# Kernel optimization log

Measured on AMD Instinct MI355X. Metric: run time of the kernel, lower is better.

Reference implementation:

```python
import jax, jax.numpy as jnp
import numpy as np
from jax import lax


def _pairwise_dist(a, b):
    # a: (T, D), b: (T, D) -> (T, T) Euclidean distances via GEMM trick
    a2 = jnp.sum(a * a, axis=-1)
    b2 = jnp.sum(b * b, axis=-1)
    sq = a2[:, None] + b2[None, :] - 2.0 * (a @ b.T)
    return jnp.sqrt(jnp.maximum(sq, 1e-12))


def _frechet(seq1, seq2):
    cost = _pairwise_dist(seq1, seq2)  # (T, T)
    ca0 = lax.cummax(cost[0])          # first row boundary: running max

    def row_step(prev, cost_row):
        # prev: ca[i-1, :]; cost_row: cost[i, :]
        c0 = jnp.maximum(prev[0], cost_row[0])  # first-column boundary

        def col_step(left, x):
            c, up, diag = x
            val = jnp.maximum(c, jnp.minimum(jnp.minimum(up, left), diag))
            return val, val

        _, rest = lax.scan(col_step, c0, (cost_row[1:], prev[1:], prev[:-1]))
        cur = jnp.concatenate([c0[None], rest])
        return cur, None

    final_row, _ = lax.scan(row_step, ca0, cost[1:])
    return final_row[-1]


def setup_inputs() -> dict:
    key = jax.random.key(0)
    k1, k2 = jax.random.split(key)
    B, T, D = 32, 1024, 64
    pred = jax.random.normal(k1, (B, T, D), dtype=jnp.float32)
    targ = jax.random.normal(k2, (B, T, D), dtype=jnp.float32)
    return {"pred": pred, "targ": targ}


def reference(pred, targ):
    dists = jax.vmap(_frechet)(pred, targ)  # (B,)
    return jnp.mean(dists)
```

## Files before the change

kernel.cpp:

```cpp
#include <hip/hip_runtime.h>
#include <hip/hip_bf16.h>

#define T_LEN 1024
#define D_DIM 64
#define BATCH 32

__global__ __launch_bounds__(256) void cost_kernel(const float* __restrict__ pred,
                                                   const float* __restrict__ targ,
                                                   float* __restrict__ cost) {
    const int b = blockIdx.z;
    const float* P = pred + (size_t)b * T_LEN * D_DIM;
    const float* T = targ + (size_t)b * T_LEN * D_DIM;
    float* C = cost + (size_t)b * T_LEN * T_LEN;
    const int row0 = blockIdx.y * 64;
    const int col0 = blockIdx.x * 64;

    __shared__ __align__(16) float ps[64][68];
    __shared__ __align__(16) float ts[64][68];
    __shared__ float p2[64], t2[64];

    const int tid = threadIdx.x;

#pragma unroll
    for (int it = 0; it < 4; it++) {
        int f = tid + 256 * it;
        int row = f >> 4;
        int kc = f & 15;
        float4 v = *(const float4*)(P + (size_t)(row0 + row) * D_DIM + 4 * kc);
        ps[4 * kc + 0][row] = v.x; ps[4 * kc + 1][row] = v.y;
        ps[4 * kc + 2][row] = v.z; ps[4 * kc + 3][row] = v.w;
        float4 w = *(const float4*)(T + (size_t)(col0 + row) * D_DIM + 4 * kc);
        ts[4 * kc + 0][row] = w.x; ts[4 * kc + 1][row] = w.y;
        ts[4 * kc + 2][row] = w.z; ts[4 * kc + 3][row] = w.w;
    }
    __syncthreads();

    if (tid < 128) {
        int idx = tid & 63;
        float s = 0.0f;
        if (tid < 64) {
#pragma unroll
            for (int k = 0; k < 64; k++) { float x = ps[k][idx]; s += x * x; }
            p2[idx] = s;
        } else {
#pragma unroll
            for (int k = 0; k < 64; k++) { float x = ts[k][idx]; s += x * x; }
            t2[idx] = s;
        }
    }
    __syncthreads();

    const int tx = tid & 15, ty = tid >> 4;
    const int r0 = 4 * ty, c0 = 4 * tx;
    float acc[4][4];
#pragma unroll
    for (int i = 0; i < 4; i++)
#pragma unroll
        for (int j = 0; j < 4; j++) acc[i][j] = 0.0f;

#pragma unroll 8
    for (int k = 0; k < 64; k++) {
        float4 a = *(const float4*)&ps[k][r0];
        float4 bb = *(const float4*)&ts[k][c0];
        float av[4] = {a.x, a.y, a.z, a.w};
        float bv[4] = {bb.x, bb.y, bb.z, bb.w};
#pragma unroll
        for (int i = 0; i < 4; i++)
#pragma unroll
            for (int j = 0; j < 4; j++) acc[i][j] += av[i] * bv[j];
    }

#pragma unroll
    for (int i = 0; i < 4; i++) {
        float4 o;
        float pa = p2[r0 + i];
        float d0 = pa + t2[c0 + 0] - 2.0f * acc[i][0];
        float d1 = pa + t2[c0 + 1] - 2.0f * acc[i][1];
        float d2 = pa + t2[c0 + 2] - 2.0f * acc[i][2];
        float d3 = pa + t2[c0 + 3] - 2.0f * acc[i][3];
        o.x = sqrtf(fmaxf(d0, 1e-12f));
        o.y = sqrtf(fmaxf(d1, 1e-12f));
        o.z = sqrtf(fmaxf(d2, 1e-12f));
        o.w = sqrtf(fmaxf(d3, 1e-12f));
        *(float4*)(C + (size_t)(row0 + r0 + i) * T_LEN + (col0 + c0)) = o;
    }
}

#define PD 8
__global__ __launch_bounds__(64) void dp_kernel(const float* __restrict__ cost,
                                                float* __restrict__ out) {
    const int b = blockIdx.x;
    const int t = threadIdx.x;
    const float INF = __builtin_inff();
    const float* C = cost + (size_t)b * T_LEN * T_LEN + 16 * t;

    float prev[16];
#pragma unroll
    for (int j = 0; j < 16; j++) prev[j] = INF;
    float right_out = INF;
    float diag_feed = INF;

    float4 pipe[PD][4];
#pragma unroll
    for (int d = 0; d < PD; d++) {
        int r = d - t; r = r < 0 ? 0 : (r > T_LEN - 1 ? T_LEN - 1 : r);
        const float4* p = (const float4*)(C + (size_t)r * T_LEN);
        pipe[d][0] = p[0]; pipe[d][1] = p[1]; pipe[d][2] = p[2]; pipe[d][3] = p[3];
    }

    const int S = T_LEN + 63;
    const int NCH = (S + PD - 1) / PD;
    int s = 0;
    for (int chunk = 0; chunk < NCH; chunk++) {
#pragma unroll
        for (int u = 0; u < PD; u++, s++) {
            int r = s - t;
            float inc = __shfl_up(right_out, 1, 64);
            float left = inc, diag = diag_feed;
            diag_feed = inc;
            if (t == 0) { left = (r == 0) ? -INF : INF; diag = INF; }
            if (r >= 0 && r < T_LEN) {
                const float* cb = (const float*)&pipe[u][0];
#pragma unroll
                for (int j = 0; j < 16; j++) {
                    float c = cb[j];
                    float up = prev[j];
                    float v = fmaxf(c, fminf(fminf(up, diag), left));
                    diag = up; left = v; prev[j] = v;
                }
                right_out = left;
            }
            int rn = s + PD - t; rn = rn < 0 ? 0 : (rn > T_LEN - 1 ? T_LEN - 1 : rn);
            const float4* p = (const float4*)(C + (size_t)rn * T_LEN);
            pipe[u][0] = p[0]; pipe[u][1] = p[1]; pipe[u][2] = p[2]; pipe[u][3] = p[3];
        }
    }
    if (t == 63) atomicAdd(out, prev[15] * (1.0f / (float)BATCH));
}

__global__ __launch_bounds__(64) void dp_fused_kernel(const float* __restrict__ pred,
                                                      const float* __restrict__ targ,
                                                      float* __restrict__ out) {
    const int b = blockIdx.x;
    const int t = threadIdx.x;
    const float INF = __builtin_inff();
    const float* P = pred + (size_t)b * T_LEN * D_DIM;
    const float* T = targ + (size_t)b * T_LEN * D_DIM + (size_t)(16 * t) * D_DIM;

    float prev[16];
#pragma unroll
    for (int j = 0; j < 16; j++) prev[j] = INF;
    float right_out = INF;
    float diag_feed = INF;

    for (int s = 0; s < T_LEN + 63; s++) {
        int r = s - t;
        float inc = __shfl_up(right_out, 1, 64);
        float left = inc, diag = diag_feed;
        diag_feed = inc;
        if (t == 0) { left = (r == 0) ? -INF : INF; diag = INF; }
        if (r >= 0 && r < T_LEN) {
            float4 pr[16];
            const float4* pp = (const float4*)(P + (size_t)r * D_DIM);
#pragma unroll
            for (int q = 0; q < 16; q++) pr[q] = pp[q];
#pragma unroll
            for (int j = 0; j < 16; j++) {
                const float4* tp = (const float4*)(T + (size_t)j * D_DIM);
                float acc = 0.0f;
#pragma unroll
                for (int q = 0; q < 16; q++) {
                    float4 tv = tp[q];
                    float dx = pr[q].x - tv.x; acc += dx * dx;
                    float dy = pr[q].y - tv.y; acc += dy * dy;
                    float dz = pr[q].z - tv.z; acc += dz * dz;
                    float dw = pr[q].w - tv.w; acc += dw * dw;
                }
                float c = sqrtf(fmaxf(acc, 1e-12f));
                float up = prev[j];
                float v = fmaxf(c, fminf(fminf(up, diag), left));
                diag = up; left = v; prev[j] = v;
            }
            right_out = left;
        }
    }
    if (t == 63) atomicAdd(out, prev[15] * (1.0f / (float)BATCH));
}

extern "C" void kernel_launch(void* const* d_in, const int* in_sizes, int n_in,
                              void* d_out, int out_size, void* d_ws, size_t ws_size,
                              hipStream_t stream) {
    const float* pred = (const float*)d_in[0];
    const float* targ = (const float*)d_in[1];
    float* out = (float*)d_out;

    hipMemsetAsync(out, 0, sizeof(float) * out_size, stream);

    const size_t per_batch = (size_t)T_LEN * T_LEN * sizeof(float);
    int bpg = (int)(ws_size / per_batch);
    if (bpg > BATCH) bpg = BATCH;

    if (bpg >= 1) {
        float* cost = (float*)d_ws;
        for (int g0 = 0; g0 < BATCH; g0 += bpg) {
            int gb = (BATCH - g0) < bpg ? (BATCH - g0) : bpg;
            dim3 grid(16, 16, gb);
            cost_kernel<<<grid, 256, 0, stream>>>(pred + (size_t)g0 * T_LEN * D_DIM,
                                                  targ + (size_t)g0 * T_LEN * D_DIM,
                                                  cost);
            dp_kernel<<<gb, 64, 0, stream>>>(cost, out);
        }
    } else {
        dp_fused_kernel<<<BATCH, 64, 0, stream>>>(pred, targ, out);
    }
}
```

Before: 309.8 us.

## Pad cost matrix with INF slack rows to remove DP boundary branches

The cost workspace is laid out with INF-filled slack rows before and after each batch, so the wavefront DP kernel can run every step without clamping row indices or checking validity. The per-cell recurrence is rewritten with fmed3 to use fewer min/max operations. The cost GEMM moves to 128x128 tiles with 8x8 register blocking and a two-chunk K loop. The cost is an extra fill kernel, a larger workspace requirement, and more register pressure in the cost kernel.

```diff
diff --git a/kernel.cpp b/kernel.cpp
--- a/kernel.cpp
+++ b/kernel.cpp
@@ -1,94 +1,188 @@
 #include <hip/hip_runtime.h>
 #include <hip/hip_bf16.h>
+#include <math.h>
 
 #define T_LEN 1024
 #define D_DIM 64
 #define BATCH 32
 
+#define SLACK_FRONT 64
+#define SLACK_BACK  72
+#define ROW_STRIDE  (T_LEN + SLACK_FRONT)
+#define PD 8
+
+__global__ __launch_bounds__(256) void fill_slack_kernel(float* __restrict__ ws) {
+    int g = blockIdx.x * 256 + threadIdx.x;
+    int b = g >> 14;
+    int off = g & 16383;
+    float4* dst = (float4*)(ws + (size_t)b * (ROW_STRIDE * T_LEN)) + off;
+    const float INF = __builtin_inff();
+    *dst = make_float4(INF, INF, INF, INF);
+}
+
 __global__ __launch_bounds__(256) void cost_kernel(const float* __restrict__ pred,
                                                    const float* __restrict__ targ,
-                                                   float* __restrict__ cost) {
+                                                   float* __restrict__ cost_base,
+                                                   unsigned long long batch_stride_f) {
     const int b = blockIdx.z;
     const float* P = pred + (size_t)b * T_LEN * D_DIM;
     const float* T = targ + (size_t)b * T_LEN * D_DIM;
-    float* C = cost + (size_t)b * T_LEN * T_LEN;
-    const int row0 = blockIdx.y * 64;
-    const int col0 = blockIdx.x * 64;
-
-    __shared__ __align__(16) float ps[64][68];
-    __shared__ __align__(16) float ts[64][68];
-    __shared__ float p2[64], t2[64];
+    float* C = cost_base + (size_t)b * batch_stride_f;
+    const int row0 = blockIdx.y * 128;
+    const int col0 = blockIdx.x * 128;
+
+    __shared__ __align__(16) float ps[32][132];
+    __shared__ __align__(16) float ts[32][132];
+    __shared__ float p2[128], t2[128];
 
     const int tid = threadIdx.x;
 
-#pragma unroll
-    for (int it = 0; it < 4; it++) {
-        int f = tid + 256 * it;
-        int row = f >> 4;
-        int kc = f & 15;
-        float4 v = *(const float4*)(P + (size_t)(row0 + row) * D_DIM + 4 * kc);
-        ps[4 * kc + 0][row] = v.x; ps[4 * kc + 1][row] = v.y;
-        ps[4 * kc + 2][row] = v.z; ps[4 * kc + 3][row] = v.w;
-        float4 w = *(const float4*)(T + (size_t)(col0 + row) * D_DIM + 4 * kc);
-        ts[4 * kc + 0][row] = w.x; ts[4 * kc + 1][row] = w.y;
-        ts[4 * kc + 2][row] = w.z; ts[4 * kc + 3][row] = w.w;
+    {
+        int r = tid & 127;
+        const float* src = (tid < 128) ? (P + (size_t)(row0 + r) * D_DIM)
+                                       : (T + (size_t)(col0 + r) * D_DIM);
+        float s = 0.0f;
+#pragma unroll
+        for (int q = 0; q < 16; q++) {
+            float4 v = ((const float4*)src)[q];
+            s += v.x * v.x + v.y * v.y + v.z * v.z + v.w * v.w;
+        }
+        if (tid < 128) p2[r] = s; else t2[r] = s;
+    }
+
+    const int lane = tid & 63, wv = tid >> 6;
+    const int TX = (lane & 7) + 8 * (wv & 1);
+    const int TY = (lane >> 3) + 8 * (wv >> 1);
+
+    float acc[8][8];
+#pragma unroll
+    for (int i = 0; i < 8; i++)
+#pragma unroll
+        for (int j = 0; j < 8; j++) acc[i][j] = 0.0f;
+
+#pragma unroll
+    for (int chunk = 0; chunk < 2; ++chunk) {
+        __syncthreads();
+#pragma unroll
+        for (int it = 0; it < 4; ++it) {
+            int idx = tid + 256 * it;
+            int row = idx >> 3;
+            int kc = idx & 7;
+            float4 v = *(const float4*)(P + (size_t)(row0 + row) * D_DIM + 32 * chunk + 4 * kc);
+            ps[4 * kc + 0][row] = v.x; ps[4 * kc + 1][row] = v.y;
+            ps[4 * kc + 2][row] = v.z; ps[4 * kc + 3][row] = v.w;
+            float4 w = *(const float4*)(T + (size_t)(col0 + row) * D_DIM + 32 * chunk + 4 * kc);
+            ts[4 * kc + 0][row] = w.x; ts[4 * kc + 1][row] = w.y;
+            ts[4 * kc + 2][row] = w.z; ts[4 * kc + 3][row] = w.w;
+        }
+        __syncthreads();
+
+#pragma unroll
+        for (int kk = 0; kk < 32; ++kk) {
+            float4 a0 = *(const float4*)&ps[kk][8 * TY];
+            float4 a1 = *(const float4*)&ps[kk][8 * TY + 4];
+            float4 b0 = *(const float4*)&ts[kk][8 * TX];
+            float4 b1 = *(const float4*)&ts[kk][8 * TX + 4];
+            float av[8] = {a0.x, a0.y, a0.z, a0.w, a1.x, a1.y, a1.z, a1.w};
+            float bv[8] = {b0.x, b0.y, b0.z, b0.w, b1.x, b1.y, b1.z, b1.w};
+#pragma unroll
+            for (int i = 0; i < 8; i++)
+#pragma unroll
+                for (int j = 0; j < 8; j++) acc[i][j] += av[i] * bv[j];
+        }
     }
     __syncthreads();
 
-    if (tid < 128) {
-        int idx = tid & 63;
-        float s = 0.0f;
-        if (tid < 64) {
-#pragma unroll
-            for (int k = 0; k < 64; k++) { float x = ps[k][idx]; s += x * x; }
-            p2[idx] = s;
-        } else {
-#pragma unroll
-            for (int k = 0; k < 64; k++) { float x = ts[k][idx]; s += x * x; }
-            t2[idx] = s;
-        }
-    }
-    __syncthreads();
-
-    const int tx = tid & 15, ty = tid >> 4;
-    const int r0 = 4 * ty, c0 = 4 * tx;
-    float acc[4][4];
-#pragma unroll
-    for (int i = 0; i < 4; i++)
-#pragma unroll
-        for (int j = 0; j < 4; j++) acc[i][j] = 0.0f;
-
-#pragma unroll 8
-    for (int k = 0; k < 64; k++) {
-        float4 a = *(const float4*)&ps[k][r0];
-        float4 bb = *(const float4*)&ts[k][c0];
-        float av[4] = {a.x, a.y, a.z, a.w};
-        float bv[4] = {bb.x, bb.y, bb.z, bb.w};
-#pragma unroll
-        for (int i = 0; i < 4; i++)
-#pragma unroll
-            for (int j = 0; j < 4; j++) acc[i][j] += av[i] * bv[j];
-    }
-
-#pragma unroll
-    for (int i = 0; i < 4; i++) {
-        float4 o;
-        float pa = p2[r0 + i];
-        float d0 = pa + t2[c0 + 0] - 2.0f * acc[i][0];
-        float d1 = pa + t2[c0 + 1] - 2.0f * acc[i][1];
-        float d2 = pa + t2[c0 + 2] - 2.0f * acc[i][2];
-        float d3 = pa + t2[c0 + 3] - 2.0f * acc[i][3];
-        o.x = sqrtf(fmaxf(d0, 1e-12f));
-        o.y = sqrtf(fmaxf(d1, 1e-12f));
-        o.z = sqrtf(fmaxf(d2, 1e-12f));
-        o.w = sqrtf(fmaxf(d3, 1e-12f));
-        *(float4*)(C + (size_t)(row0 + r0 + i) * T_LEN + (col0 + c0)) = o;
-    }
-}
-
-#define PD 8
-__global__ __launch_bounds__(64) void dp_kernel(const float* __restrict__ cost,
-                                                float* __restrict__ out) {
+#pragma unroll
+    for (int i = 0; i < 8; i++) {
+        float pa = p2[8 * TY + i];
+        float o[8];
+#pragma unroll
+        for (int j = 0; j < 8; j++) {
+            float d = pa + t2[8 * TX + j] - 2.0f * acc[i][j];
+            o[j] = sqrtf(fmaxf(d, 1e-12f));
+        }
+        float* dst = C + (size_t)(row0 + 8 * TY + i) * T_LEN + col0 + 8 * TX;
+        ((float4*)dst)[0] = make_float4(o[0], o[1], o[2], o[3]);
+        ((float4*)dst)[1] = make_float4(o[4], o[5], o[6], o[7]);
+    }
+}
+
+__global__ __launch_bounds__(64, 1) void dp_kernel_nb(const float* __restrict__ cost,
+                                                      float* __restrict__ out) {
+    const int b = blockIdx.x;
+    const int t = threadIdx.x;
+    const float INF = __builtin_inff();
+    const float* Cl = cost + ((size_t)SLACK_FRONT + (size_t)b * ROW_STRIDE) * T_LEN + 16 * t;
+
+    float prev[16];
+#pragma unroll
+    for (int j = 0; j < 16; j++) prev[j] = INF;
+    float right_out = INF;
+    float diag_feed = INF;
+    float lane0_left = -INF;
+
+    float4 pipe[PD][4];
+    const float* ptr[PD];
+#pragma unroll
+    for (int d = 0; d < PD; d++) {
+        const float* p = Cl + (ptrdiff_t)(d - t) * T_LEN;
+        const float4* p4 = (const float4*)p;
+        pipe[d][0] = p4[0]; pipe[d][1] = p4[1]; pipe[d][2] = p4[2]; pipe[d][3] = p4[3];
+        ptr[d] = Cl + (ptrdiff_t)(d + PD - t) * T_LEN;
+    }
+
+    for (int chunk = 0; chunk < 135; ++chunk) {
+#pragma unroll
+        for (int u = 0; u < PD; u++) {
+            float inc = __shfl_up(right_out, 1, 64);
+            float left = (t == 0) ? lane0_left : inc;
+            float diag = (t == 0) ? INF : diag_feed;
+            diag_feed = inc;
+            const float* cb = (const float*)&pipe[u][0];
+#pragma unroll
+            for (int j = 0; j < 16; j++) {
+                float c = cb[j];
+                float e = fminf(prev[j], diag);
+                float h = fmaxf(e, c);
+                float v = __builtin_amdgcn_fmed3f(c, h, left);
+                diag = prev[j];
+                prev[j] = v;
+                left = v;
+            }
+            right_out = left;
+            lane0_left = INF;
+            const float4* p4 = (const float4*)ptr[u];
+            pipe[u][0] = p4[0]; pipe[u][1] = p4[1]; pipe[u][2] = p4[2]; pipe[u][3] = p4[3];
+            ptr[u] += PD * T_LEN;
+        }
+    }
+#pragma unroll
+    for (int u = 0; u < 7; u++) {
+        float inc = __shfl_up(right_out, 1, 64);
+        float left = (t == 0) ? lane0_left : inc;
+        float diag = (t == 0) ? INF : diag_feed;
+        diag_feed = inc;
+        const float* cb = (const float*)&pipe[u][0];
+#pragma unroll
+        for (int j = 0; j < 16; j++) {
+            float c = cb[j];
+            float e = fminf(prev[j], diag);
+            float h = fmaxf(e, c);
+            float v = __builtin_amdgcn_fmed3f(c, h, left);
+            diag = prev[j];
+            prev[j] = v;
+            left = v;
+        }
+        right_out = left;
+        lane0_left = INF;
+    }
+
+    if (t == 63) atomicAdd(out, prev[15] * (1.0f / (float)BATCH));
+}
+
+__global__ __launch_bounds__(64, 1) void dp_kernel_clamped(const float* __restrict__ cost,
+                                                           float* __restrict__ out) {
     const int b = blockIdx.x;
     const int t = threadIdx.x;
     const float INF = __builtin_inff();
@@ -124,9 +218,12 @@
 #pragma unroll
                 for (int j = 0; j < 16; j++) {
                     float c = cb[j];
-                    float up = prev[j];
-                    float v = fmaxf(c, fminf(fminf(up, diag), left));
-                    diag = up; left = v; prev[j] = v;
+                    float e = fminf(prev[j], diag);
+                    float h = fmaxf(e, c);
+                    float v = __builtin_amdgcn_fmed3f(c, h, left);
+                    diag = prev[j];
+                    prev[j] = v;
+                    left = v;
                 }
                 right_out = left;
             }
@@ -177,9 +274,12 @@
                     float dw = pr[q].w - tv.w; acc += dw * dw;
                 }
                 float c = sqrtf(fmaxf(acc, 1e-12f));
-                float up = prev[j];
-                float v = fmaxf(c, fminf(fminf(up, diag), left));
-                diag = up; left = v; prev[j] = v;
+                float e = fminf(prev[j], diag);
+                float h = fmaxf(e, c);
+                float v = __builtin_amdgcn_fmed3f(c, h, left);
+                diag = prev[j];
+                prev[j] = v;
+                left = v;
             }
             right_out = left;
         }
@@ -196,21 +296,33 @@
 
     hipMemsetAsync(out, 0, sizeof(float) * out_size, stream);
 
-    const size_t per_batch = (size_t)T_LEN * T_LEN * sizeof(float);
-    int bpg = (int)(ws_size / per_batch);
-    if (bpg > BATCH) bpg = BATCH;
-
-    if (bpg >= 1) {
-        float* cost = (float*)d_ws;
-        for (int g0 = 0; g0 < BATCH; g0 += bpg) {
-            int gb = (BATCH - g0) < bpg ? (BATCH - g0) : bpg;
-            dim3 grid(16, 16, gb);
-            cost_kernel<<<grid, 256, 0, stream>>>(pred + (size_t)g0 * T_LEN * D_DIM,
-                                                  targ + (size_t)g0 * T_LEN * D_DIM,
-                                                  cost);
-            dp_kernel<<<gb, 64, 0, stream>>>(cost, out);
-        }
+    const size_t need_strided = ((size_t)BATCH * ROW_STRIDE + SLACK_BACK) * (size_t)T_LEN * sizeof(float);
+    const size_t per_batch_compact = (size_t)T_LEN * T_LEN * sizeof(float);
+
+    if (ws_size >= need_strided) {
+        float* ws = (float*)d_ws;
+        fill_slack_kernel<<<2048, 256, 0, stream>>>(ws);
+        float* cost_base = ws + (size_t)SLACK_FRONT * T_LEN;
+        dim3 grid(8, 8, BATCH);
+        cost_kernel<<<grid, 256, 0, stream>>>(pred, targ, cost_base,
+                                              (unsigned long long)ROW_STRIDE * T_LEN);
+        dp_kernel_nb<<<BATCH, 64, 0, stream>>>(ws, out);
     } else {
-        dp_fused_kernel<<<BATCH, 64, 0, stream>>>(pred, targ, out);
-    }
-}
+        int bpg = (int)(ws_size / per_batch_compact);
+        if (bpg > BATCH) bpg = BATCH;
+        if (bpg >= 1) {
+            float* cost = (float*)d_ws;
+            for (int g0 = 0; g0 < BATCH; g0 += bpg) {
+                int gb = (BATCH - g0) < bpg ? (BATCH - g0) : bpg;
+                dim3 grid(8, 8, gb);
+                cost_kernel<<<grid, 256, 0, stream>>>(pred + (size_t)g0 * T_LEN * D_DIM,
+                                                      targ + (size_t)g0 * T_LEN * D_DIM,
+                                                      cost,
+                                                      (unsigned long long)T_LEN * T_LEN);
+                dp_kernel_clamped<<<gb, 64, 0, stream>>>(cost, out);
+            }
+        } else {
+            dp_fused_kernel<<<BATCH, 64, 0, stream>>>(pred, targ, out);
+        }
+    }
+}
```

Result: slower. 393.1 us (+26.9%).
